# Kernel tuning notes

Hardware: AMD Instinct MI355X
Metric: run time of the kernel (lower is better)

## Reference

```python
import jax, jax.numpy as jnp
import numpy as np

N = 100_000      # nodes
E = 1_600_000    # edges (avg degree 16)
D_IN = 128
D_H = 128
D_P = 128
D_OUT = 64


def setup_inputs() -> dict:
    key = jax.random.key(0)
    ks = jax.random.split(key, 10)
    x = jax.random.normal(ks[0], (N, D_IN), dtype=jnp.float32)
    edge_index = jax.random.randint(ks[1], (2, E), 0, N, dtype=jnp.int64)
    # Mix_Pass layer 0: Linear(in->hidden, bias=False) + separate bias (zero-init)
    W1 = jax.random.normal(ks[2], (D_H, D_IN), dtype=jnp.float32) * 0.05
    b1 = jnp.zeros((D_H,), dtype=jnp.float32)
    # Mix_Pass layer 1: hidden->hidden
    W2 = jax.random.normal(ks[3], (D_H, D_H), dtype=jnp.float32) * 0.05
    b2 = jnp.zeros((D_H,), dtype=jnp.float32)
    # projection MLP
    fcW1 = jax.random.normal(ks[4], (D_P, D_H), dtype=jnp.float32) * 0.05
    fcb1 = jnp.zeros((D_P,), dtype=jnp.float32)
    fcW2 = jax.random.normal(ks[5], (D_OUT, D_P), dtype=jnp.float32) * 0.05
    fcb2 = jnp.zeros((D_OUT,), dtype=jnp.float32)
    return dict(x=x, edge_index=edge_index, W1=W1, b1=b1, W2=W2, b2=b2,
                fcW1=fcW1, fcb1=fcb1, fcW2=fcW2, fcb2=fcb2)


def _gcn_norm_with_self_loops(edge_index, n_nodes):
    # add_self_loops then gcn_norm (sym, improved=False, loops already added)
    loop = jnp.arange(n_nodes, dtype=edge_index.dtype)
    row = jnp.concatenate([edge_index[0], loop])  # source
    col = jnp.concatenate([edge_index[1], loop])  # target
    ew = jnp.ones(row.shape[0], dtype=jnp.float32)
    deg = jax.ops.segment_sum(ew, col, num_segments=n_nodes)
    dinv = jnp.where(deg > 0, jax.lax.rsqrt(deg), 0.0)
    return row, col, dinv[row] * ew * dinv[col]


def _mix_pass(z, W, b, row, col, ew, n_nodes):
    z = z @ W.T                                   # [N, out]
    msg = ew[:, None] * z[row]                    # gather source feats, scale
    out = jax.ops.segment_sum(msg, col, num_segments=n_nodes)  # scatter-add
    return out + b


def reference(x, edge_index, W1, b1, W2, b2, fcW1, fcb1, fcW2, fcb2):
    n_nodes = x.shape[0]
    row, col, ew = _gcn_norm_with_self_loops(edge_index, n_nodes)
    # dropout is identity in eval mode
    z = jax.nn.relu(_mix_pass(x, W1, b1, row, col, ew, n_nodes))
    zs = _mix_pass(z, W2, b2, row, col, ew, n_nodes)
    # project: elu(fc1) -> log_softmax(fc2)
    h = jax.nn.elu(zs @ fcW1.T + fcb1)
    res = jax.nn.log_softmax(h @ fcW2.T + fcb2, axis=1)
    return zs, res
```

## Files before the change

kernel.cpp:

```cpp
#include <hip/hip_runtime.h>
#include <hip/hip_bf16.h>

typedef __bf16 bf16_t;
typedef bf16_t bf16x8 __attribute__((ext_vector_type(8)));
typedef bf16_t bf16x4 __attribute__((ext_vector_type(4)));
typedef float f32x4 __attribute__((ext_vector_type(4)));
typedef float f32x2 __attribute__((ext_vector_type(2)));

#define DEG_CAP 64
#define BKT_SHIFT 7
#define BKT_NODES 128
#define BKT_CAP 3328
#define EPT 16
#define LDW 136

__device__ __forceinline__ void cvt4(const float* __restrict__ s, bf16_t* __restrict__ d, int i) {
    f32x4 v = ((const f32x4*)s)[i];
    bf16x4 o;
#pragma unroll
    for (int j = 0; j < 4; ++j) o[j] = (bf16_t)v[j];
    ((bf16x4*)d)[i] = o;
}

__global__ void setup_k(const float* W1f, bf16_t* W1b,
                        const float* W2f, bf16_t* W2b,
                        const float* fW1f, bf16_t* fW1b,
                        const float* fW2f, bf16_t* fW2b,
                        int* gbcnt, int NB, int* yzero) {
    int i = blockIdx.x * blockDim.x + threadIdx.x;
    if (i < 4096) { cvt4(W1f, W1b, i); return; }
    i -= 4096;
    if (i < 4096) { cvt4(W2f, W2b, i); return; }
    i -= 4096;
    if (i < 4096) { cvt4(fW1f, fW1b, i); return; }
    i -= 4096;
    if (i < 2048) { cvt4(fW2f, fW2b, i); return; }
    i -= 2048;
    if (i < NB) { gbcnt[i] = 0; return; }
    i -= NB;
    if (i < 64) yzero[i] = 0;
}

__global__ __launch_bounds__(256) void bucket_scatter_k(const int* __restrict__ ei,
                                                        int* __restrict__ gbcnt,
                                                        unsigned* __restrict__ grec,
                                                        int E, int N) {
    __shared__ int hist[1024];
    __shared__ int base[1024];
    const int tid = threadIdx.x;
    const int NB = (N + BKT_NODES - 1) >> BKT_SHIFT;
    for (int i = tid; i < NB; i += 256) hist[i] = 0;
    __syncthreads();

    const int wave = tid >> 6, lane = tid & 63;
    const int e0 = blockIdx.x * (256 * EPT) + wave * (64 * EPT) + lane;
    const bool i64 = (ei[1] == 0) & (ei[3] == 0) & (ei[5] == 0) & (ei[7] == 0);

    unsigned rec[EPT];
    int lof[EPT];
    int bk[EPT];
#pragma unroll
    for (int j = 0; j < EPT; ++j) {
        int e = e0 + j * 64;
        bk[j] = -1;
        if (e < E) {
            int r, c;
            if (i64) { r = ei[2 * e]; c = ei[2 * E + 2 * e]; }
            else     { r = ei[e];     c = ei[E + e]; }
            r = ((unsigned)r < (unsigned)N) ? r : 0;
            c = ((unsigned)c < (unsigned)N) ? c : 0;
            int b = c >> BKT_SHIFT;
            rec[j] = ((unsigned)r << BKT_SHIFT) | (unsigned)(c & (BKT_NODES - 1));
            bk[j] = b;
            lof[j] = atomicAdd(&hist[b], 1);
        }
    }
    __syncthreads();
    for (int i = tid; i < NB; i += 256)
        base[i] = hist[i] ? atomicAdd(&gbcnt[i], hist[i]) : 0;
    __syncthreads();
#pragma unroll
    for (int j = 0; j < EPT; ++j) {
        if (bk[j] >= 0) {
            int pos = base[bk[j]] + lof[j];
            if (pos < BKT_CAP)
                grec[(size_t)bk[j] * BKT_CAP + pos] = rec[j];
        }
    }
}

__global__ __launch_bounds__(256) void bucket_place_k(const int* __restrict__ gbcnt,
                                                      const unsigned* __restrict__ grec,
                                                      int* __restrict__ cnt,
                                                      int* __restrict__ srcx, int N) {
    __shared__ int lcnt[BKT_NODES];
    const int b = blockIdx.x, tid = threadIdx.x;
    if (tid < BKT_NODES) lcnt[tid] = 0;
    __syncthreads();
    int ne = gbcnt[b];
    if (ne > BKT_CAP) ne = BKT_CAP;
    const unsigned* rp = grec + (size_t)b * BKT_CAP;
    const int node0 = b << BKT_SHIFT;
    for (int i = tid; i < ne; i += 256) {
        unsigned rec = rp[i];
        int cl = rec & (BKT_NODES - 1);
        int r  = rec >> BKT_SHIFT;
        int p = atomicAdd(&lcnt[cl], 1);
        if (p < DEG_CAP) srcx[(size_t)(node0 + cl) * DEG_CAP + p] = r;
    }
    __syncthreads();
    int node = node0 + tid;
    if (tid < BKT_NODES && node < N) {
        int c = lcnt[tid];
        cnt[node] = c;
        int cc = (c < DEG_CAP) ? c : DEG_CAP;
        int pe = (cc + 15) & ~15;
        if (pe < 16) pe = 16;
        if (pe > DEG_CAP) pe = DEG_CAP;
        int* s = srcx + (size_t)node * DEG_CAP;
        for (int p = cc; p < pe; ++p) s[p] = N;
    }
}

template <int RELU, int WF32>
__global__ __launch_bounds__(256) void gather_k(const bf16_t* __restrict__ Y,
                                                const int* __restrict__ cnt,
                                                const int* __restrict__ srcx,
                                                const float* __restrict__ bias,
                                                bf16_t* __restrict__ out,
                                                float* __restrict__ out2, int n) {
    int node = blockIdx.x * 4 + (threadIdx.x >> 6);
    if (node >= n) return;
    const int lane = threadIdx.x & 63;
    const int l16 = lane & 15;
    const int quad = lane >> 4;
    const int* sl = srcx + (size_t)node * DEG_CAP + quad * 4;
    const bf16_t* Yl = Y + l16 * 8;

    int4 sq = *(const int4*)sl;
    bf16x8 ys = *(const bf16x8*)(Yl + (size_t)node * 128);
    int c = cnt[node];
    float di = rsqrtf((float)c + 1.0f);
    int cg = (c < DEG_CAP) ? c : DEG_CAP;
    int nb = (cg + 15) & ~15;

    f32x2 acc[4];
#pragma unroll
    for (int p = 0; p < 4; ++p) acc[p] = (f32x2){0.f, 0.f};

#define ACC_ROW(s)                                                             \
    {                                                                          \
        bf16x8 yv = *(const bf16x8*)(Yl + (size_t)(s) * 128);                  \
        uint4 u = *(const uint4*)&yv;                                          \
        acc[0] += (f32x2){__uint_as_float(u.x << 16),                          \
                          __uint_as_float(u.x & 0xFFFF0000u)};                 \
        acc[1] += (f32x2){__uint_as_float(u.y << 16),                          \
                          __uint_as_float(u.y & 0xFFFF0000u)};                 \
        acc[2] += (f32x2){__uint_as_float(u.z << 16),                          \
                          __uint_as_float(u.z & 0xFFFF0000u)};                 \
        acc[3] += (f32x2){__uint_as_float(u.w << 16),                          \
                          __uint_as_float(u.w & 0xFFFF0000u)};                 \
    }

    ACC_ROW(sq.x); ACC_ROW(sq.y); ACC_ROW(sq.z); ACC_ROW(sq.w);
    for (int e = 16; e < nb; e += 16) {
        int4 s2 = *(const int4*)(sl + e);
        ACC_ROW(s2.x); ACC_ROW(s2.y); ACC_ROW(s2.z); ACC_ROW(s2.w);
    }
#undef ACC_ROW

    float a[8];
#pragma unroll
    for (int p = 0; p < 4; ++p) { a[2 * p] = acc[p][0]; a[2 * p + 1] = acc[p][1]; }
#pragma unroll
    for (int j = 0; j < 8; ++j) {
        a[j] += __shfl_xor(a[j], 16);
        a[j] += __shfl_xor(a[j], 32);
    }

    f32x4 b0 = ((const f32x4*)bias)[l16 * 2];
    f32x4 b1 = ((const f32x4*)bias)[l16 * 2 + 1];
    float v[8];
#pragma unroll
    for (int j = 0; j < 8; ++j) {
        float bb = (j < 4) ? b0[j & 3] : b1[j & 3];
        v[j] = di * ((float)ys[j] + a[j]) + bb;
        if (RELU) v[j] = fmaxf(v[j], 0.f);
    }

    if (quad == 0) {
        bf16x8 o;
#pragma unroll
        for (int j = 0; j < 8; ++j) o[j] = (bf16_t)v[j];
        *(bf16x8*)(out + (size_t)node * 128 + l16 * 8) = o;
    }
    if (WF32) {
        if (quad == 1) {
            f32x4 w = {v[0], v[1], v[2], v[3]};
            *(f32x4*)(out2 + (size_t)node * 128 + l16 * 8) = w;
        } else if (quad == 2) {
            f32x4 w = {v[4], v[5], v[6], v[7]};
            *(f32x4*)(out2 + (size_t)node * 128 + l16 * 8 + 4) = w;
        }
    }
}

template <int OC, int MT, int AF32>
__global__ __launch_bounds__(256) void gemm_k(const void* __restrict__ Av,
                                              const bf16_t* __restrict__ W,
                                              const int* __restrict__ cnt,
                                              bf16_t* __restrict__ out, int nrows) {
    const int lane = threadIdx.x & 63;
    const int wave = threadIdx.x >> 6;
    const int l16 = lane & 15;
    const int quad = lane >> 4;
    constexpr int NT = OC / 16;
    const int ntiles = (nrows + 15) >> 4;
    const int t0 = (blockIdx.x * 4 + wave) * MT;
    if (t0 >= ntiles) return;

    f32x4 acc[MT][NT];
#pragma unroll
    for (int mt = 0; mt < MT; ++mt)
#pragma unroll
        for (int n = 0; n < NT; ++n) acc[mt][n] = (f32x4){0.f, 0.f, 0.f, 0.f};

    const bf16_t* arow[MT];
    const float* afrow[MT];
#pragma unroll
    for (int mt = 0; mt < MT; ++mt) {
        int r = t0 * 16 + mt * 16 + l16;
        if (r > nrows - 1) r = nrows - 1;
        if (AF32) afrow[mt] = (const float*)Av + (size_t)r * 128 + quad * 8;
        else      arow[mt]  = (const bf16_t*)Av + (size_t)r * 128 + quad * 8;
    }
    const bf16_t* wrow = W + (size_t)l16 * 128 + quad * 8;

#pragma unroll
    for (int kt = 0; kt < 4; ++kt) {
        bf16x8 a[MT];
#pragma unroll
        for (int mt = 0; mt < MT; ++mt) {
            if (AF32) {
                f32x4 lo = *(const f32x4*)(afrow[mt] + kt * 32);
                f32x4 hi = *(const f32x4*)(afrow[mt] + kt * 32 + 4);
#pragma unroll
                for (int j = 0; j < 4; ++j) {
                    a[mt][j] = (bf16_t)lo[j];
                    a[mt][j + 4] = (bf16_t)hi[j];
                }
            } else {
                a[mt] = *(const bf16x8*)(arow[mt] + kt * 32);
            }
        }
#pragma unroll
        for (int n = 0; n < NT; ++n) {
            bf16x8 b = *(const bf16x8*)(wrow + (size_t)n * 2048 + kt * 32);
#pragma unroll
            for (int mt = 0; mt < MT; ++mt)
                acc[mt][n] = __builtin_amdgcn_mfma_f32_16x16x32_bf16(a[mt], b, acc[mt][n], 0, 0, 0);
        }
    }

#pragma unroll
    for (int mt = 0; mt < MT; ++mt) {
        int m0 = (t0 + mt) * 16;
        if (m0 >= nrows) break;
#pragma unroll
        for (int r = 0; r < 4; ++r) {
            int row = m0 + quad * 4 + r;
            if (row < nrows) {
                float sc = rsqrtf((float)cnt[row] + 1.0f);
#pragma unroll
                for (int n = 0; n < NT; ++n)
                    out[(size_t)row * OC + n * 16 + l16] = (bf16_t)(sc * acc[mt][n][r]);
            }
        }
    }
}

__global__ __launch_bounds__(256) void head_k(const bf16_t* __restrict__ A,
                                              const bf16_t* __restrict__ W1,
                                              const float* __restrict__ b1,
                                              const bf16_t* __restrict__ W2,
                                              const float* __restrict__ b2,
                                              float* __restrict__ outf, int nrows) {
    __shared__ bf16_t hl[4][16 * LDW];
    const int lane = threadIdx.x & 63;
    const int wave = threadIdx.x >> 6;
    const int l16 = lane & 15;
    const int quad = lane >> 4;
    const int ntiles = (nrows + 15) >> 4;
    int t = blockIdx.x * 4 + wave;
    const bool live = t < ntiles;
    if (!live) t = ntiles - 1;
    const int m0 = t * 16;

    f32x4 acc[8];
#pragma unroll
    for (int n = 0; n < 8; ++n) acc[n] = (f32x4){0.f, 0.f, 0.f, 0.f};
    int r0 = m0 + l16;
    if (r0 > nrows - 1) r0 = nrows - 1;
    const bf16_t* arow = A + (size_t)r0 * 128 + quad * 8;
    const bf16_t* wrow = W1 + (size_t)l16 * 128 + quad * 8;
#pragma unroll
    for (int kt = 0; kt < 4; ++kt) {
        bf16x8 a = *(const bf16x8*)(arow + kt * 32);
#pragma unroll
        for (int n = 0; n < 8; ++n) {
            bf16x8 b = *(const bf16x8*)(wrow + (size_t)n * 2048 + kt * 32);
            acc[n] = __builtin_amdgcn_mfma_f32_16x16x32_bf16(a, b, acc[n], 0, 0, 0);
        }
    }
    bf16_t* hw = hl[wave];
#pragma unroll
    for (int n = 0; n < 8; ++n) {
        float bb = b1[n * 16 + l16];
#pragma unroll
        for (int r = 0; r < 4; ++r) {
            float v = acc[n][r] + bb;
            v = (v > 0.0f) ? v : (expf(v) - 1.0f);
            hw[(quad * 4 + r) * LDW + n * 16 + l16] = (bf16_t)v;
        }
    }
    __syncthreads();

    f32x4 acc2[4];
#pragma unroll
    for (int n = 0; n < 4; ++n) acc2[n] = (f32x4){0.f, 0.f, 0.f, 0.f};
    const bf16_t* hrow = hw + l16 * LDW + quad * 8;
    const bf16_t* wrow2 = W2 + (size_t)l16 * 128 + quad * 8;
#pragma unroll
    for (int kt = 0; kt < 4; ++kt) {
        bf16x8 a = *(const bf16x8*)(hrow + kt * 32);
#pragma unroll
        for (int n = 0; n < 4; ++n) {
            bf16x8 b = *(const bf16x8*)(wrow2 + (size_t)n * 2048 + kt * 32);
            acc2[n] = __builtin_amdgcn_mfma_f32_16x16x32_bf16(a, b, acc2[n], 0, 0, 0);
        }
    }
#pragma unroll
    for (int r = 0; r < 4; ++r) {
        float v[4];
#pragma unroll
        for (int n = 0; n < 4; ++n) v[n] = acc2[n][r] + b2[n * 16 + l16];
        float mx = v[0];
#pragma unroll
        for (int n = 1; n < 4; ++n) mx = fmaxf(mx, v[n]);
#pragma unroll
        for (int m = 8; m >= 1; m >>= 1) mx = fmaxf(mx, __shfl_xor(mx, m));
        float s = 0.0f;
#pragma unroll
        for (int n = 0; n < 4; ++n) s += expf(v[n] - mx);
#pragma unroll
        for (int m = 8; m >= 1; m >>= 1) s += __shfl_xor(s, m);
        float lse = mx + logf(s);
        int row = m0 + quad * 4 + r;
        if (live && row < nrows)
#pragma unroll
            for (int n = 0; n < 4; ++n)
                outf[(size_t)row * 64 + n * 16 + l16] = v[n] - lse;
    }
}

extern "C" void kernel_launch(void* const* d_in, const int* in_sizes, int n_in,
                              void* d_out, int out_size, void* d_ws, size_t ws_size,
                              hipStream_t stream) {
    const float* xf    = (const float*)d_in[0];
    const int*   ei    = (const int*)d_in[1];
    const float* W1f   = (const float*)d_in[2];
    const float* b1f   = (const float*)d_in[3];
    const float* W2f   = (const float*)d_in[4];
    const float* b2f   = (const float*)d_in[5];
    const float* fcW1f = (const float*)d_in[6];
    const float* fcb1f = (const float*)d_in[7];
    const float* fcW2f = (const float*)d_in[8];
    const float* fcb2f = (const float*)d_in[9];

    const int N = in_sizes[0] / 128;
    const int E = in_sizes[1] / 2;
    const int NB = (N + BKT_NODES - 1) >> BKT_SHIFT;

    float* zs_out  = (float*)d_out;
    float* res_out = (float*)d_out + (size_t)N * 128;

    char* ws = (char*)d_ws;
    size_t o = 0;
    auto carve = [&](size_t bytes) { void* p = ws + o; o = (o + bytes + 255) & ~255UL; return p; };
    int*      cnt   = (int*)carve((size_t)N * 4);
    int*      srcx  = (int*)carve((size_t)N * DEG_CAP * 4);
    bf16_t*   Xbf   = (bf16_t*)carve((size_t)N * 128 * 2);
    bf16_t*   Ybf   = (bf16_t*)carve((size_t)(N + 1) * 128 * 2);
    bf16_t*   W1b   = (bf16_t*)carve(128 * 128 * 2);
    bf16_t*   W2b   = (bf16_t*)carve(128 * 128 * 2);
    bf16_t*   fW1b  = (bf16_t*)carve(128 * 128 * 2);
    bf16_t*   fW2b  = (bf16_t*)carve(64 * 128 * 2);
    unsigned* grec  = (unsigned*)carve((size_t)NB * BKT_CAP * 4);
    int*      gbcnt = (int*)carve((size_t)NB * 4);

    const int B = 256;
    const int ntiles = (N + 15) / 16;
    const int gblocks = (ntiles + 7) / 8;
    const int hblocks = (ntiles + 3) / 4;
    const int nodeblocks = (N + 3) / 4;
    const int nsetup = 4096 * 3 + 2048 + NB + 64;
    const int ablocks = (E + 256 * EPT - 1) / (256 * EPT);

    setup_k<<<(nsetup + B - 1) / B, B, 0, stream>>>(W1f, W1b, W2f, W2b,
                                                    fcW1f, fW1b, fcW2f, fW2b, gbcnt, NB,
                                                    (int*)(Ybf + (size_t)N * 128));
    bucket_scatter_k<<<ablocks, B, 0, stream>>>(ei, gbcnt, grec, E, N);
    bucket_place_k<<<NB, B, 0, stream>>>(gbcnt, grec, cnt, srcx, N);

    gemm_k<128, 2, 1><<<gblocks, B, 0, stream>>>((const void*)xf, W1b, cnt, Ybf, N);
    gather_k<1, 0><<<nodeblocks, B, 0, stream>>>(Ybf, cnt, srcx, b1f, Xbf, nullptr, N);

    gemm_k<128, 2, 0><<<gblocks, B, 0, stream>>>((const void*)Xbf, W2b, cnt, Ybf, N);
    gather_k<0, 1><<<nodeblocks, B, 0, stream>>>(Ybf, cnt, srcx, b2f, Xbf, zs_out, N);

    head_k<<<hblocks, B, 0, stream>>>(Xbf, fW1b, fcb1f, fW2b, fcb2f, res_out, N);
}
```

Before: 392.8 us.

## Store GEMM output in feature-sliced layout and gather one slice per XCD

The GEMM now writes Y as eight 16-feature slices, each a contiguous [N+1][16] array, instead of row-major 128-wide rows. The gather kernel is split per slice, with the slice index taken from blockIdx & 7. Under round-robin block dispatch across the eight XCDs, each XCD's L2 then only needs to cache one roughly 3 MB slice rather than the whole feature matrix, cutting random-gather misses. The cost is 8x more blocks, each rereading the neighbor index list and doing narrow 32-byte row reads, and the padding-row zeroing is adjusted to the new layout.

After: 739.1 us. 88.1% more time.

```diff
diff --git a/kernel.cpp b/kernel.cpp
--- a/kernel.cpp
+++ b/kernel.cpp
@@ -4,6 +4,7 @@
 typedef __bf16 bf16_t;
 typedef bf16_t bf16x8 __attribute__((ext_vector_type(8)));
 typedef bf16_t bf16x4 __attribute__((ext_vector_type(4)));
+typedef bf16_t bf16x2v __attribute__((ext_vector_type(2)));
 typedef float f32x4 __attribute__((ext_vector_type(4)));
 typedef float f32x2 __attribute__((ext_vector_type(2)));
 
@@ -26,7 +27,7 @@
                         const float* W2f, bf16_t* W2b,
                         const float* fW1f, bf16_t* fW1b,
                         const float* fW2f, bf16_t* fW2b,
-                        int* gbcnt, int NB, int* yzero) {
+                        int* gbcnt, int NB, int* yzero, int srow) {
     int i = blockIdx.x * blockDim.x + threadIdx.x;
     if (i < 4096) { cvt4(W1f, W1b, i); return; }
     i -= 4096;
@@ -38,7 +39,10 @@
     i -= 2048;
     if (i < NB) { gbcnt[i] = 0; return; }
     i -= NB;
-    if (i < 64) yzero[i] = 0;
+    if (i < 64) {
+        int sl = i >> 3, d = i & 7;
+        yzero[((size_t)sl * srow + (srow - 1)) * 8 + d] = 0;
+    }
 }
 
 __global__ __launch_bounds__(256) void bucket_scatter_k(const int* __restrict__ ei,
@@ -123,85 +127,58 @@
 }
 
 template <int RELU, int WF32>
-__global__ __launch_bounds__(256) void gather_k(const bf16_t* __restrict__ Y,
+__global__ __launch_bounds__(256) void gather_s(const bf16_t* __restrict__ Yt,
                                                 const int* __restrict__ cnt,
                                                 const int* __restrict__ srcx,
                                                 const float* __restrict__ bias,
                                                 bf16_t* __restrict__ out,
-                                                float* __restrict__ out2, int n) {
-    int node = blockIdx.x * 4 + (threadIdx.x >> 6);
+                                                float* __restrict__ out2,
+                                                int n, int srow) {
+    const int s = blockIdx.x & 7;
+    const int node = (blockIdx.x >> 3) * 4 + (threadIdx.x >> 6);
     if (node >= n) return;
     const int lane = threadIdx.x & 63;
-    const int l16 = lane & 15;
-    const int quad = lane >> 4;
-    const int* sl = srcx + (size_t)node * DEG_CAP + quad * 4;
-    const bf16_t* Yl = Y + l16 * 8;
-
-    int4 sq = *(const int4*)sl;
-    bf16x8 ys = *(const bf16x8*)(Yl + (size_t)node * 128);
+    const int g = lane >> 3;
+    const int fl = lane & 7;
+    const bf16_t* Ys = Yt + (size_t)s * srow * 16;
+    const int* sl = srcx + (size_t)node * DEG_CAP;
+
+    unsigned selfd = *(const unsigned*)(Ys + (size_t)node * 16 + fl * 2);
+    int s0 = sl[g];
     int c = cnt[node];
     float di = rsqrtf((float)c + 1.0f);
     int cg = (c < DEG_CAP) ? c : DEG_CAP;
-    int nb = (cg + 15) & ~15;
-
-    f32x2 acc[4];
-#pragma unroll
-    for (int p = 0; p < 4; ++p) acc[p] = (f32x2){0.f, 0.f};
-
-#define ACC_ROW(s)                                                             \
-    {                                                                          \
-        bf16x8 yv = *(const bf16x8*)(Yl + (size_t)(s) * 128);                  \
-        uint4 u = *(const uint4*)&yv;                                          \
-        acc[0] += (f32x2){__uint_as_float(u.x << 16),                          \
-                          __uint_as_float(u.x & 0xFFFF0000u)};                 \
-        acc[1] += (f32x2){__uint_as_float(u.y << 16),                          \
-                          __uint_as_float(u.y & 0xFFFF0000u)};                 \
-        acc[2] += (f32x2){__uint_as_float(u.z << 16),                          \
-                          __uint_as_float(u.z & 0xFFFF0000u)};                 \
-        acc[3] += (f32x2){__uint_as_float(u.w << 16),                          \
-                          __uint_as_float(u.w & 0xFFFF0000u)};                 \
-    }
-
-    ACC_ROW(sq.x); ACC_ROW(sq.y); ACC_ROW(sq.z); ACC_ROW(sq.w);
-    for (int e = 16; e < nb; e += 16) {
-        int4 s2 = *(const int4*)(sl + e);
-        ACC_ROW(s2.x); ACC_ROW(s2.y); ACC_ROW(s2.z); ACC_ROW(s2.w);
-    }
-#undef ACC_ROW
-
-    float a[8];
-#pragma unroll
-    for (int p = 0; p < 4; ++p) { a[2 * p] = acc[p][0]; a[2 * p + 1] = acc[p][1]; }
-#pragma unroll
-    for (int j = 0; j < 8; ++j) {
-        a[j] += __shfl_xor(a[j], 16);
-        a[j] += __shfl_xor(a[j], 32);
-    }
-
-    f32x4 b0 = ((const f32x4*)bias)[l16 * 2];
-    f32x4 b1 = ((const f32x4*)bias)[l16 * 2 + 1];
-    float v[8];
-#pragma unroll
-    for (int j = 0; j < 8; ++j) {
-        float bb = (j < 4) ? b0[j & 3] : b1[j & 3];
-        v[j] = di * ((float)ys[j] + a[j]) + bb;
-        if (RELU) v[j] = fmaxf(v[j], 0.f);
-    }
-
-    if (quad == 0) {
-        bf16x8 o;
-#pragma unroll
-        for (int j = 0; j < 8; ++j) o[j] = (bf16_t)v[j];
-        *(bf16x8*)(out + (size_t)node * 128 + l16 * 8) = o;
-    }
-    if (WF32) {
-        if (quad == 1) {
-            f32x4 w = {v[0], v[1], v[2], v[3]};
-            *(f32x4*)(out2 + (size_t)node * 128 + l16 * 8) = w;
-        } else if (quad == 2) {
-            f32x4 w = {v[4], v[5], v[6], v[7]};
-            *(f32x4*)(out2 + (size_t)node * 128 + l16 * 8 + 4) = w;
-        }
+    int nb = (cg + 7) & ~7;
+
+    unsigned d0 = *(const unsigned*)(Ys + (size_t)s0 * 16 + fl * 2);
+    float a0 = __uint_as_float(d0 << 16);
+    float a1 = __uint_as_float(d0 & 0xFFFF0000u);
+    for (int e = 8; e < nb; e += 8) {
+        int sv = sl[e + g];
+        unsigned d = *(const unsigned*)(Ys + (size_t)sv * 16 + fl * 2);
+        a0 += __uint_as_float(d << 16);
+        a1 += __uint_as_float(d & 0xFFFF0000u);
+    }
+    a0 += __shfl_xor(a0, 8);  a1 += __shfl_xor(a1, 8);
+    a0 += __shfl_xor(a0, 16); a1 += __shfl_xor(a1, 16);
+    a0 += __shfl_xor(a0, 32); a1 += __shfl_xor(a1, 32);
+    a0 += __uint_as_float(selfd << 16);
+    a1 += __uint_as_float(selfd & 0xFFFF0000u);
+
+    float2 bb = *(const float2*)(bias + s * 16 + fl * 2);
+    float v0 = di * a0 + bb.x;
+    float v1 = di * a1 + bb.y;
+    if (RELU) { v0 = fmaxf(v0, 0.f); v1 = fmaxf(v1, 0.f); }
+
+    if (g == 0) {
+        bf16x2v o;
+        o[0] = (bf16_t)v0;
+        o[1] = (bf16_t)v1;
+        *(bf16x2v*)(out + (size_t)node * 128 + s * 16 + fl * 2) = o;
+    }
+    if (WF32 && g == 1) {
+        float2 w = {v0, v1};
+        *(float2*)(out2 + (size_t)node * 128 + s * 16 + fl * 2) = w;
     }
 }
 
@@ -209,7 +186,8 @@
 __global__ __launch_bounds__(256) void gemm_k(const void* __restrict__ Av,
                                               const bf16_t* __restrict__ W,
                                               const int* __restrict__ cnt,
-                                              bf16_t* __restrict__ out, int nrows) {
+                                              bf16_t* __restrict__ out, int nrows,
+                                              int srow) {
     const int lane = threadIdx.x & 63;
     const int wave = threadIdx.x >> 6;
     const int l16 = lane & 15;
@@ -273,7 +251,7 @@
                 float sc = rsqrtf((float)cnt[row] + 1.0f);
 #pragma unroll
                 for (int n = 0; n < NT; ++n)
-                    out[(size_t)row * OC + n * 16 + l16] = (bf16_t)(sc * acc[mt][n][r]);
+                    out[((size_t)n * srow + row) * 16 + l16] = (bf16_t)(sc * acc[mt][n][r]);
             }
         }
     }
@@ -380,6 +358,7 @@
     const int N = in_sizes[0] / 128;
     const int E = in_sizes[1] / 2;
     const int NB = (N + BKT_NODES - 1) >> BKT_SHIFT;
+    const int srow = N + 1;
 
     float* zs_out  = (float*)d_out;
     float* res_out = (float*)d_out + (size_t)N * 128;
@@ -390,7 +369,7 @@
     int*      cnt   = (int*)carve((size_t)N * 4);
     int*      srcx  = (int*)carve((size_t)N * DEG_CAP * 4);
     bf16_t*   Xbf   = (bf16_t*)carve((size_t)N * 128 * 2);
-    bf16_t*   Ybf   = (bf16_t*)carve((size_t)(N + 1) * 128 * 2);
+    bf16_t*   Ybf   = (bf16_t*)carve((size_t)srow * 128 * 2);
     bf16_t*   W1b   = (bf16_t*)carve(128 * 128 * 2);
     bf16_t*   W2b   = (bf16_t*)carve(128 * 128 * 2);
     bf16_t*   fW1b  = (bf16_t*)carve(128 * 128 * 2);
@@ -402,21 +381,21 @@
     const int ntiles = (N + 15) / 16;
     const int gblocks = (ntiles + 7) / 8;
     const int hblocks = (ntiles + 3) / 4;
-    const int nodeblocks = (N + 3) / 4;
+    const int sblocks = 8 * ((N + 3) / 4);
     const int nsetup = 4096 * 3 + 2048 + NB + 64;
     const int ablocks = (E + 256 * EPT - 1) / (256 * EPT);
 
     setup_k<<<(nsetup + B - 1) / B, B, 0, stream>>>(W1f, W1b, W2f, W2b,
                                                     fcW1f, fW1b, fcW2f, fW2b, gbcnt, NB,
-                                                    (int*)(Ybf + (size_t)N * 128));
+                                                    (int*)Ybf, srow);
     bucket_scatter_k<<<ablocks, B, 0, stream>>>(ei, gbcnt, grec, E, N);
     bucket_place_k<<<NB, B, 0, stream>>>(gbcnt, grec, cnt, srcx, N);
 
-    gemm_k<128, 2, 1><<<gblocks, B, 0, stream>>>((const void*)xf, W1b, cnt, Ybf, N);
-    gather_k<1, 0><<<nodeblocks, B, 0, stream>>>(Ybf, cnt, srcx, b1f, Xbf, nullptr, N);
-
-    gemm_k<128, 2, 0><<<gblocks, B, 0, stream>>>((const void*)Xbf, W2b, cnt, Ybf, N);
-    gather_k<0, 1><<<nodeblocks, B, 0, stream>>>(Ybf, cnt, srcx, b2f, Xbf, zs_out, N);
+    gemm_k<128, 2, 1><<<gblocks, B, 0, stream>>>((const void*)xf, W1b, cnt, Ybf, N, srow);
+    gather_s<1, 0><<<sblocks, B, 0, stream>>>(Ybf, cnt, srcx, b1f, Xbf, nullptr, N, srow);
+
+    gemm_k<128, 2, 0><<<gblocks, B, 0, stream>>>((const void*)Xbf, W2b, cnt, Ybf, N, srow);
+    gather_s<0, 1><<<sblocks, B, 0, stream>>>(Ybf, cnt, srcx, b2f, Xbf, zs_out, N, srow);
 
     head_k<<<hblocks, B, 0, stream>>>(Xbf, fW1b, fcb1f, fW2b, fcb2f, res_out, N);
 }
```
